# Performance work log

Hardware: AMD Instinct MI355X
Metric: run time of the kernel (lower is better)

## Reference

```python
import jax, jax.numpy as jnp
import numpy as np

N_NODES = 50000
N_EDGES = 800000
IN_FEAT = 512
OUT_FEAT = 128


def multispike(x):
    return jnp.floor(jnp.clip(4.0 * x, 0.0, 4.0) + 0.5) / 4.0


def setup_inputs() -> dict:
    key = jax.random.key(0)
    k1, k2, k3, k4, k5 = jax.random.split(key, 5)
    feat = jax.random.normal(k1, (N_NODES, IN_FEAT), dtype=jnp.float32)
    # Xavier-uniform-like init for the weight parameter
    limit = np.sqrt(6.0 / (IN_FEAT + OUT_FEAT)).astype(np.float32)
    weight = jax.random.uniform(k2, (IN_FEAT, OUT_FEAT), dtype=jnp.float32,
                                minval=-limit, maxval=limit)
    rows = jnp.sort(jax.random.randint(k3, (N_EDGES,), 0, N_NODES, dtype=jnp.int32))
    cols = jax.random.randint(k4, (N_EDGES,), 0, N_NODES, dtype=jnp.int32)
    edge_weight = jax.random.uniform(k5, (N_EDGES,), dtype=jnp.float32)
    return {"feat": feat, "weight": weight, "rows": rows, "cols": cols,
            "edge_weight": edge_weight}


def reference(feat, weight, rows, cols, edge_weight):
    # x = feat @ W                     [N, out_feat]
    x = jnp.matmul(feat, weight)
    # x = spmm(adj, x): out[i] = sum_{e: rows[e]==i} w_e * x[cols[e]]
    edge_feats = edge_weight[:, None] * x[cols]          # [E, out_feat]
    x = jax.ops.segment_sum(edge_feats, rows, num_segments=N_NODES)
    # quantized multi-spike activation
    return multispike(x)
```

## Files before the change

kernel.cpp:

```cpp
#include <hip/hip_runtime.h>

#define N_NODES 50000
#define N_EDGES 800000
#define IN_FEAT 512
#define OUT_FEAT 128


__device__ __forceinline__ float multispike(float a) {
    return floorf(fminf(fmaxf(4.0f * a, 0.0f), 4.0f) + 0.5f) * 0.25f;
}

__global__ __launch_bounds__(256) void gemm_kernel(const float* __restrict__ A,
                                                   const float* __restrict__ B,
                                                   float* __restrict__ C, int M) {
    __shared__ float As[32][68];

    const int tid = threadIdx.x;
    const int tx = tid & 31;
    const int ty = tid >> 5;
    const int block_m = blockIdx.x * 64;

    const float4* __restrict__ B4 = (const float4*)B;

    float acc[8][4];
#pragma unroll
    for (int i = 0; i < 8; i++)
#pragma unroll
        for (int j = 0; j < 4; j++) acc[i][j] = 0.0f;

    for (int k0 = 0; k0 < IN_FEAT; k0 += 32) {
#pragma unroll
        for (int i = 0; i < 2; i++) {
            int f = tid + i * 256;
            int r = f >> 3;
            int kq = (f & 7) << 2;
            int gm = block_m + r;
            float4 v = make_float4(0.f, 0.f, 0.f, 0.f);
            if (gm < M) v = *(const float4*)(A + (size_t)gm * IN_FEAT + k0 + kq);
            As[kq + 0][r] = v.x;
            As[kq + 1][r] = v.y;
            As[kq + 2][r] = v.z;
            As[kq + 3][r] = v.w;
        }
        __syncthreads();

#pragma unroll
        for (int k = 0; k < 32; k++) {
            float4 b = B4[(size_t)(k0 + k) * 32 + tx];
            float4 a0 = *(const float4*)&As[k][ty * 8];
            float4 a1 = *(const float4*)&As[k][ty * 8 + 4];
            float av[8] = {a0.x, a0.y, a0.z, a0.w, a1.x, a1.y, a1.z, a1.w};
            float bv[4] = {b.x, b.y, b.z, b.w};
#pragma unroll
            for (int i = 0; i < 8; i++)
#pragma unroll
                for (int j = 0; j < 4; j++)
                    acc[i][j] = fmaf(av[i], bv[j], acc[i][j]);
        }
        __syncthreads();
    }

#pragma unroll
    for (int i = 0; i < 8; i++) {
        int gm = block_m + ty * 8 + i;
        if (gm < M) {
            float4 v = make_float4(acc[i][0], acc[i][1], acc[i][2], acc[i][3]);
            *(float4*)(C + (size_t)gm * OUT_FEAT + tx * 4) = v;
        }
    }
}

__global__ __launch_bounds__(256) void rowptr_kernel(const int* __restrict__ rows,
                                                     int* __restrict__ row_ptr) {
    int i = blockIdx.x * blockDim.x + threadIdx.x;
    if (i > N_NODES) return;
    int lo = 0, hi = N_EDGES;
    while (lo < hi) {
        int mid = (lo + hi) >> 1;
        if (rows[mid] < i) lo = mid + 1; else hi = mid;
    }
    row_ptr[i] = lo;
}

__global__ __launch_bounds__(256) void spmm_kernel(const float* __restrict__ x,
                                                   const int* __restrict__ cols,
                                                   const float* __restrict__ ew,
                                                   const int* __restrict__ row_ptr,
                                                   float* __restrict__ out) {
    const int wave = threadIdx.x >> 6;
    const int lane = threadIdx.x & 63;
    const int r = blockIdx.x * 4 + wave;
    if (r >= N_NODES) return;

    const int e0 = row_ptr[r];
    const int e1 = row_ptr[r + 1];
    const float2* __restrict__ x2 = (const float2*)x;

    float accx = 0.0f, accy = 0.0f;
    int e = e0;
    for (; e + 8 <= e1; e += 8) {
        int c[8];
        float w[8];
        float2 v[8];
#pragma unroll
        for (int j = 0; j < 8; j++) {
            c[j] = cols[e + j];
            w[j] = ew[e + j];
        }
#pragma unroll
        for (int j = 0; j < 8; j++) {
            v[j] = x2[(size_t)c[j] * 64 + lane];
        }
#pragma unroll
        for (int j = 0; j < 8; j++) {
            accx = fmaf(w[j], v[j].x, accx);
            accy = fmaf(w[j], v[j].y, accy);
        }
    }
    for (; e < e1; e++) {
        int c = cols[e];
        float w = ew[e];
        float2 v = x2[(size_t)c * 64 + lane];
        accx = fmaf(w, v.x, accx);
        accy = fmaf(w, v.y, accy);
    }
    float2* out2 = (float2*)out;
    out2[(size_t)r * 64 + lane] = make_float2(multispike(accx), multispike(accy));
}

extern "C" void kernel_launch(void* const* d_in, const int* in_sizes, int n_in,
                              void* d_out, int out_size, void* d_ws, size_t ws_size,
                              hipStream_t stream) {
    const float* feat = (const float*)d_in[0];
    const float* weight = (const float*)d_in[1];
    const int* rows = (const int*)d_in[2];
    const int* cols = (const int*)d_in[3];
    const float* ew = (const float*)d_in[4];
    float* out = (float*)d_out;

    float* x = (float*)d_ws;
    int* row_ptr = (int*)((char*)d_ws + (size_t)N_NODES * OUT_FEAT * sizeof(float));

    rowptr_kernel<<<(N_NODES + 256) / 256, 256, 0, stream>>>(rows, row_ptr);
    gemm_kernel<<<(N_NODES + 63) / 64, 256, 0, stream>>>(feat, weight, x, N_NODES);
    spmm_kernel<<<(N_NODES + 3) / 4, 256, 0, stream>>>(x, cols, ew, row_ptr, out);
}
```

Measured before the change: 336.0 us.

## Drop LDS staging in GEMM and read A rows directly from global

```diff
diff --git a/kernel.cpp b/kernel.cpp
--- a/kernel.cpp
+++ b/kernel.cpp
@@ -13,14 +13,22 @@
 __global__ __launch_bounds__(256) void gemm_kernel(const float* __restrict__ A,
                                                    const float* __restrict__ B,
                                                    float* __restrict__ C, int M) {
-    __shared__ float As[32][68];
-
     const int tid = threadIdx.x;
     const int tx = tid & 31;
     const int ty = tid >> 5;
-    const int block_m = blockIdx.x * 64;
+    const int m0 = blockIdx.x * 64 + ty * 8;
 
+    const float4* __restrict__ A4 = (const float4*)A;
     const float4* __restrict__ B4 = (const float4*)B;
+
+    const size_t o0 = (size_t)min(m0 + 0, M - 1) * 128;
+    const size_t o1 = (size_t)min(m0 + 1, M - 1) * 128;
+    const size_t o2 = (size_t)min(m0 + 2, M - 1) * 128;
+    const size_t o3 = (size_t)min(m0 + 3, M - 1) * 128;
+    const size_t o4 = (size_t)min(m0 + 4, M - 1) * 128;
+    const size_t o5 = (size_t)min(m0 + 5, M - 1) * 128;
+    const size_t o6 = (size_t)min(m0 + 6, M - 1) * 128;
+    const size_t o7 = (size_t)min(m0 + 7, M - 1) * 128;
 
     float acc[8][4];
 #pragma unroll
@@ -28,41 +36,52 @@
 #pragma unroll
         for (int j = 0; j < 4; j++) acc[i][j] = 0.0f;
 
-    for (int k0 = 0; k0 < IN_FEAT; k0 += 32) {
-#pragma unroll
-        for (int i = 0; i < 2; i++) {
-            int f = tid + i * 256;
-            int r = f >> 3;
-            int kq = (f & 7) << 2;
-            int gm = block_m + r;
-            float4 v = make_float4(0.f, 0.f, 0.f, 0.f);
-            if (gm < M) v = *(const float4*)(A + (size_t)gm * IN_FEAT + k0 + kq);
-            As[kq + 0][r] = v.x;
-            As[kq + 1][r] = v.y;
-            As[kq + 2][r] = v.z;
-            As[kq + 3][r] = v.w;
-        }
-        __syncthreads();
+#pragma unroll 2
+    for (int kb = 0; kb < 128; kb++) {
+        float4 b0 = B4[(size_t)(kb * 4 + 0) * 32 + tx];
+        float4 b1 = B4[(size_t)(kb * 4 + 1) * 32 + tx];
+        float4 b2 = B4[(size_t)(kb * 4 + 2) * 32 + tx];
+        float4 b3 = B4[(size_t)(kb * 4 + 3) * 32 + tx];
+        float4 a0 = A4[o0 + kb];
+        float4 a1 = A4[o1 + kb];
+        float4 a2 = A4[o2 + kb];
+        float4 a3 = A4[o3 + kb];
+        float4 a4 = A4[o4 + kb];
+        float4 a5 = A4[o5 + kb];
+        float4 a6 = A4[o6 + kb];
+        float4 a7 = A4[o7 + kb];
 
-#pragma unroll
-        for (int k = 0; k < 32; k++) {
-            float4 b = B4[(size_t)(k0 + k) * 32 + tx];
-            float4 a0 = *(const float4*)&As[k][ty * 8];
-            float4 a1 = *(const float4*)&As[k][ty * 8 + 4];
-            float av[8] = {a0.x, a0.y, a0.z, a0.w, a1.x, a1.y, a1.z, a1.w};
-            float bv[4] = {b.x, b.y, b.z, b.w};
-#pragma unroll
-            for (int i = 0; i < 8; i++)
-#pragma unroll
-                for (int j = 0; j < 4; j++)
-                    acc[i][j] = fmaf(av[i], bv[j], acc[i][j]);
-        }
-        __syncthreads();
+#define ROW_FMA(i, av)                                              \
+        acc[i][0] = fmaf(av.x, b0.x, acc[i][0]);                    \
+        acc[i][1] = fmaf(av.x, b0.y, acc[i][1]);                    \
+        acc[i][2] = fmaf(av.x, b0.z, acc[i][2]);                    \
+        acc[i][3] = fmaf(av.x, b0.w, acc[i][3]);                    \
+        acc[i][0] = fmaf(av.y, b1.x, acc[i][0]);                    \
+        acc[i][1] = fmaf(av.y, b1.y, acc[i][1]);                    \
+        acc[i][2] = fmaf(av.y, b1.z, acc[i][2]);                    \
+        acc[i][3] = fmaf(av.y, b1.w, acc[i][3]);                    \
+        acc[i][0] = fmaf(av.z, b2.x, acc[i][0]);                    \
+        acc[i][1] = fmaf(av.z, b2.y, acc[i][1]);                    \
+        acc[i][2] = fmaf(av.z, b2.z, acc[i][2]);                    \
+        acc[i][3] = fmaf(av.z, b2.w, acc[i][3]);                    \
+        acc[i][0] = fmaf(av.w, b3.x, acc[i][0]);                    \
+        acc[i][1] = fmaf(av.w, b3.y, acc[i][1]);                    \
+        acc[i][2] = fmaf(av.w, b3.z, acc[i][2]);                    \
+        acc[i][3] = fmaf(av.w, b3.w, acc[i][3]);
+        ROW_FMA(0, a0)
+        ROW_FMA(1, a1)
+        ROW_FMA(2, a2)
+        ROW_FMA(3, a3)
+        ROW_FMA(4, a4)
+        ROW_FMA(5, a5)
+        ROW_FMA(6, a6)
+        ROW_FMA(7, a7)
+#undef ROW_FMA
     }
 
 #pragma unroll
     for (int i = 0; i < 8; i++) {
-        int gm = block_m + ty * 8 + i;
+        int gm = m0 + i;
         if (gm < M) {
             float4 v = make_float4(acc[i][0], acc[i][1], acc[i][2], acc[i][3]);
             *(float4*)(C + (size_t)gm * OUT_FEAT + tx * 4) = v;
```

Result: slower. 495.3 us (+47.4%).
